# Kernel optimization log

Hardware: AMD Instinct MI355X
Metric: run time of the kernel (lower is better)

Reference implementation:

```python
import jax, jax.numpy as jnp
import numpy as np

D = 1024
H = 16
HS = 64

def setup_inputs() -> dict:
    key = jax.random.key(0)
    ks = jax.random.split(key, 9)
    s = 0.02
    x = jax.random.normal(ks[0], (2, 4096, D), dtype=jnp.float32)
    Wq = jax.random.normal(ks[1], (H, D, HS), dtype=jnp.float32) * s
    Wk = jax.random.normal(ks[2], (H, D, HS), dtype=jnp.float32) * s
    Wv = jax.random.normal(ks[3], (H, D, HS), dtype=jnp.float32) * s
    bq = jax.random.normal(ks[4], (H, HS), dtype=jnp.float32) * s
    bk = jax.random.normal(ks[5], (H, HS), dtype=jnp.float32) * s
    bv = jax.random.normal(ks[6], (H, HS), dtype=jnp.float32) * s
    Wp = jax.random.normal(ks[7], (D, D), dtype=jnp.float32) * s
    bp = jax.random.normal(ks[8], (D,), dtype=jnp.float32) * s
    return {"x": x, "Wq": Wq, "Wk": Wk, "Wv": Wv, "bq": bq, "bk": bk, "bv": bv, "Wp": Wp, "bp": bp}

def reference(x, Wq, Wk, Wv, bq, bk, bv, Wp, bp):
    B, T, _ = x.shape
    # per-head projections, stacked over heads: [B, H, T, HS]
    q = jnp.einsum('btd,hde->bhte', x, Wq) + bq[None, :, None, :]
    k = jnp.einsum('btd,hde->bhte', x, Wk) + bk[None, :, None, :]
    v = jnp.einsum('btd,hde->bhte', x, Wv) + bv[None, :, None, :]
    scale = 1.0 / jnp.sqrt(jnp.float32(HS))
    scores = jnp.einsum('bhte,bhse->bhts', q, k) * scale  # [B,H,T,T]
    causal = jnp.tril(jnp.ones((T, T), dtype=bool))
    scores = jnp.where(causal[None, None, :, :], scores, -jnp.inf)
    attn = jax.nn.softmax(scores, axis=-1)
    out = jnp.einsum('bhts,bhse->bhte', attn, v)  # [B,H,T,HS]
    # concat heads along last dim (head order preserved)
    out = out.transpose(0, 2, 1, 3).reshape(B, T, H * HS)
    return out @ Wp + bp
```

## Files before the change

kernel.cpp:

```cpp
#include <hip/hip_runtime.h>
#include <hip/hip_bf16.h>
#include <stdint.h>


typedef __bf16 bf16x8 __attribute__((ext_vector_type(8)));
typedef float f32x4 __attribute__((ext_vector_type(4)));
typedef float f32x16 __attribute__((ext_vector_type(16)));
typedef __attribute__((address_space(1))) void gvoid_t;
typedef __attribute__((address_space(3))) void lvoid_t;

using hbf = __hip_bfloat16;

#define QSCALE (0.125f * 1.44269504088896f)

static __device__ __forceinline__ void gload_lds16(const void* g, void* l) {
  __builtin_amdgcn_global_load_lds((gvoid_t*)g, (lvoid_t*)l, 16, 0, 0);
}

static __device__ __forceinline__ uint16_t b2u(float x) {
  hbf h = __float2bfloat16(x);
  return *reinterpret_cast<uint16_t*>(&h);
}

static __device__ __forceinline__ uint32_t cvtpk(float lo, float hi) {
  uint32_t r;
  asm("v_cvt_pk_bf16_f32 %0, %1, %2" : "=v"(r) : "v"(lo), "v"(hi));
  return r;
}

static __device__ __forceinline__ void pl32swap(uint32_t& x, uint32_t& y) {
  asm volatile("v_permlane32_swap_b32 %0, %1" : "+v"(x), "+v"(y));
}

static __device__ __forceinline__ float max3f(float a, float b, float c) {
  return fmaxf(fmaxf(a, b), c);
}


__global__ void k_cvt_all(const float* __restrict__ x,
                          const float* __restrict__ Wq, const float* __restrict__ Wk,
                          const float* __restrict__ Wv,
                          const float* __restrict__ bq, const float* __restrict__ bk,
                          const float* __restrict__ bv,
                          const float* __restrict__ Wp,
                          hbf* __restrict__ xb, hbf* __restrict__ Wt,
                          hbf* __restrict__ Wpt, float* __restrict__ biasc) {
  const int b = blockIdx.x, tid = threadIdx.x;
  if (b < 8192) {
    int i = (b * 256 + tid) * 4;
    float4 v = *reinterpret_cast<const float4*>(x + i);
    hbf h[4] = {__float2bfloat16(v.x), __float2bfloat16(v.y),
                __float2bfloat16(v.z), __float2bfloat16(v.w)};
    *reinterpret_cast<ushort4*>(xb + i) = *reinterpret_cast<ushort4*>(h);
  } else if (b < 20480) {
    int idx = (b - 8192) * 256 + tid;
    int d = idx & 1023, r = idx >> 10;
    int m = r >> 10, rem = r & 1023;
    int h = rem >> 6, e = rem & 63;
    const float* W = (m == 0) ? Wq : (m == 1) ? Wk : Wv;
    float v = W[(h << 10 | d) * 64 + e];
    if (m == 0) v *= QSCALE;
    Wt[idx] = __float2bfloat16(v);
  } else if (b < 24576) {
    int idx = (b - 20480) * 256 + tid;
    int o = idx >> 10, d = idx & 1023;
    Wpt[idx] = __float2bfloat16(Wp[(d << 10) + o]);
  } else {
    int r = (b - 24576) * 256 + tid;
    int m = r >> 10, rem = r & 1023;
    const float* bsrc = (m == 0) ? bq : (m == 1) ? bk : bv;
    float v = bsrc[rem];
    if (m == 0) v *= QSCALE;
    biasc[r] = v;
  }
}


__global__ __launch_bounds__(256) void k_gemm_qkv(
    const hbf* __restrict__ A, const hbf* __restrict__ Bw,
    const float* __restrict__ biasc, hbf* __restrict__ qkv) {
  __shared__ __align__(16) hbf sA[128 * 64];
  __shared__ __align__(16) hbf sB[128 * 64];
  const int tid = threadIdx.x;
  const int lane = tid & 63, wid = tid >> 6;
  int wg = blockIdx.y * 64 + blockIdx.x;
  wg = (wg & 7) * 192 + (wg >> 3);
  const int m0 = (wg & 63) * 128, n0 = (wg >> 6) * 128;
  const int g = lane >> 4, cl = lane & 15;

  const f32x4 fz = {0.f, 0.f, 0.f, 0.f};
  f32x4 acc[4][4];
#pragma unroll
  for (int a = 0; a < 4; ++a)
#pragma unroll
    for (int b = 0; b < 4; ++b) acc[a][b] = fz;

  const int srow = wid * 32 + (lane >> 3);
  const int scol = (lane & 7) * 8;

  for (int kt = 0; kt < 16; ++kt) {
    const int k0 = kt * 64;
#pragma unroll
    for (int t = 0; t < 4; ++t) {
      const int r = srow + t * 8;
      gload_lds16(A + (size_t)(m0 + r) * 1024 + k0 + scol, sA + (wid * 32 + t * 8) * 64);
      gload_lds16(Bw + (size_t)(n0 + r) * 1024 + k0 + scol, sB + (wid * 32 + t * 8) * 64);
    }
    __syncthreads();
#pragma unroll
    for (int ks = 0; ks < 2; ++ks) {
      const int ko = ks * 32 + g * 8;
      bf16x8 af[4], bfr[4];
#pragma unroll
      for (int rt = 0; rt < 4; ++rt)
        af[rt] = *reinterpret_cast<const bf16x8*>(sA + ((wid & 1) * 64 + rt * 16 + cl) * 64 + ko);
#pragma unroll
      for (int ct = 0; ct < 4; ++ct)
        bfr[ct] = *reinterpret_cast<const bf16x8*>(sB + ((wid >> 1) * 64 + ct * 16 + cl) * 64 + ko);
#pragma unroll
      for (int rt = 0; rt < 4; ++rt)
#pragma unroll
        for (int ct = 0; ct < 4; ++ct)
          acc[rt][ct] = __builtin_amdgcn_mfma_f32_16x16x32_bf16(af[rt], bfr[ct], acc[rt][ct], 0, 0, 0);
    }
    __syncthreads();
  }

#pragma unroll
  for (int rt = 0; rt < 4; ++rt)
#pragma unroll
    for (int ct = 0; ct < 4; ++ct) {
      const int colg = n0 + (wid >> 1) * 64 + ct * 16 + cl;
      const int mi = colg >> 10, rem = colg & 1023;
      const int h = rem >> 6, e = rem & 63;
      const float bi = biasc[colg];
      if (mi == 2) {
        const int t0 = m0 + (wid & 1) * 64 + rt * 16 + g * 4;
        const int b = t0 >> 12, t = t0 & 4095;
        ushort4 o;
        o.x = b2u(acc[rt][ct][0] + bi);
        o.y = b2u(acc[rt][ct][1] + bi);
        o.z = b2u(acc[rt][ct][2] + bi);
        o.w = b2u(acc[rt][ct][3] + bi);
        *reinterpret_cast<ushort4*>(
            qkv + (size_t)64 * 262144 + (size_t)(b * 16 + h) * 262144 + (size_t)e * 4096 + t) = o;
      } else {
#pragma unroll
        for (int i = 0; i < 4; ++i) {
          const int rowg = m0 + (wid & 1) * 64 + rt * 16 + g * 4 + i;
          const int b = rowg >> 12, t = rowg & 4095;
          qkv[(((size_t)mi * 32 + b * 16 + h) * 4096 + t) * 64 + e] =
              __float2bfloat16(acc[rt][ct][i] + bi);
        }
      }
    }
}


__global__ __launch_bounds__(256) void k_flash(
    const hbf* __restrict__ qkv, hbf* __restrict__ attn) {
  __shared__ __align__(16) __bf16 sK[2][64 * 64];
  __shared__ __align__(16) __bf16 sV[2][64 * 64];
  const int tid = threadIdx.x, lane = tid & 63, wq = tid >> 6;
  const int h = lane >> 5, r31 = lane & 31;
  const int bh = blockIdx.x;
  const int qtb = (int)gridDim.y - 1 - (int)blockIdx.y;
  const int q0 = qtb * 128;
  const int ntile = 2 * qtb + 2;
  const hbf* Q  = qkv + (size_t)bh * 262144;
  const hbf* Kp = qkv + (size_t)(32 + bh) * 262144;
  const hbf* Vp = qkv + (size_t)(64 + bh) * 262144;
  const float NEG_INF = -__builtin_inff();

  const int koff = (wq * 16 + (lane >> 3)) * 64 + (((lane & 7) ^ (lane >> 3)) * 8);
  const int voff = (wq * 16 + (lane >> 3)) * 4096 + (((lane & 7) ^ (lane >> 3)) * 8);

  const int qrow = q0 + wq * 32 + r31;
  bf16x8 aq[4];
#pragma unroll
  for (int ks = 0; ks < 4; ++ks)
    aq[ks] = *reinterpret_cast<const bf16x8*>(Q + (size_t)qrow * 64 + ks * 16 + h * 8);

  f32x16 accO[2];
#pragma unroll
  for (int et = 0; et < 2; ++et)
#pragma unroll
    for (int i = 0; i < 16; ++i) accO[et][i] = 0.f;
  float mrow = NEG_INF, lrow = 0.f;

  gload_lds16(Kp + koff,         &sK[0][wq * 1024]);
  gload_lds16(Kp + koff + 512,   &sK[0][wq * 1024 + 512]);
  gload_lds16(Vp + voff,         &sV[0][wq * 1024]);
  gload_lds16(Vp + voff + 32768, &sV[0][wq * 1024 + 512]);
  __syncthreads();

  const int qmaxw = q0 + wq * 32 + 31;
  int buf = 0;
  for (int jt = 0; jt < ntile; ++jt) {
    if (jt < ntile - 1) {
      const hbf* Kg = Kp + (size_t)(jt + 1) * 4096;
      gload_lds16(Kg + koff,       &sK[buf ^ 1][wq * 1024]);
      gload_lds16(Kg + koff + 512, &sK[buf ^ 1][wq * 1024 + 512]);
      const hbf* Vg = Vp + (jt + 1) * 64;
      gload_lds16(Vg + voff,         &sV[buf ^ 1][wq * 1024]);
      gload_lds16(Vg + voff + 32768, &sV[buf ^ 1][wq * 1024 + 512]);
    }

    if (64 * jt <= qmaxw) {
      const __bf16* sKb = sK[buf];
      const __bf16* sVb = sV[buf];

      f32x16 accS[2];
      __builtin_amdgcn_s_setprio(1);
#pragma unroll
      for (int t = 0; t < 2; ++t) {
        f32x16 s;
#pragma unroll
        for (int i = 0; i < 16; ++i) s[i] = 0.f;
#pragma unroll
        for (int ks = 0; ks < 4; ++ks) {
          bf16x8 ak = *reinterpret_cast<const bf16x8*>(
              sKb + (t * 32 + r31) * 64 + (((2 * ks + h) ^ (r31 & 7)) * 8));
          s = __builtin_amdgcn_mfma_f32_32x32x16_bf16(ak, aq[ks], s, 0, 0, 0);
        }
        accS[t] = s;
      }
      __builtin_amdgcn_s_setprio(0);

      if (64 * jt + 63 > q0 + wq * 32) {
#pragma unroll
        for (int t = 0; t < 2; ++t)
#pragma unroll
          for (int i = 0; i < 16; ++i) {
            const int kvg = 64 * jt + 32 * t + (i & 3) + 8 * (i >> 2) + 4 * h;
            if (kvg > qrow) accS[t][i] = NEG_INF;
          }
      }

      float g0 = max3f(accS[0][0], accS[0][1], accS[0][2]);
      float g1 = max3f(accS[0][3], accS[0][4], accS[0][5]);
      float g2 = max3f(accS[0][6], accS[0][7], accS[0][8]);
      float g3 = max3f(accS[0][9], accS[0][10], accS[0][11]);
      float g4 = max3f(accS[0][12], accS[0][13], accS[0][14]);
      float g5 = max3f(accS[0][15], accS[1][0], accS[1][1]);
      float g6 = max3f(accS[1][2], accS[1][3], accS[1][4]);
      float g7 = max3f(accS[1][5], accS[1][6], accS[1][7]);
      float g8 = max3f(accS[1][8], accS[1][9], accS[1][10]);
      float g9 = max3f(accS[1][11], accS[1][12], accS[1][13]);
      float gA = fmaxf(accS[1][14], accS[1][15]);
      float h0 = max3f(g0, g1, g2);
      float h1 = max3f(g3, g4, g5);
      float h2 = max3f(g6, g7, g8);
      float h3 = fmaxf(g9, gA);
      float pmax = fmaxf(max3f(h0, h1, h2), h3);
      pmax = fmaxf(pmax, __shfl_xor(pmax, 32));

      if (!__all(pmax - mrow <= 8.f)) {
        const float mn = fmaxf(mrow, pmax);
        const float corr = __builtin_amdgcn_exp2f(mrow - mn);
        mrow = mn;
        lrow *= corr;
#pragma unroll
        for (int et = 0; et < 2; ++et)
#pragma unroll
          for (int i = 0; i < 16; ++i) accO[et][i] *= corr;
      }

#pragma unroll
      for (int t = 0; t < 2; ++t)
#pragma unroll
        for (int i = 0; i < 16; ++i)
          accS[t][i] = __builtin_amdgcn_exp2f(accS[t][i] - mrow);
      float s0 = (accS[0][0] + accS[0][1]) + (accS[0][2] + accS[0][3]);
      float s1 = (accS[0][4] + accS[0][5]) + (accS[0][6] + accS[0][7]);
      float s2 = (accS[0][8] + accS[0][9]) + (accS[0][10] + accS[0][11]);
      float s3 = (accS[0][12] + accS[0][13]) + (accS[0][14] + accS[0][15]);
      float s4 = (accS[1][0] + accS[1][1]) + (accS[1][2] + accS[1][3]);
      float s5 = (accS[1][4] + accS[1][5]) + (accS[1][6] + accS[1][7]);
      float s6 = (accS[1][8] + accS[1][9]) + (accS[1][10] + accS[1][11]);
      float s7 = (accS[1][12] + accS[1][13]) + (accS[1][14] + accS[1][15]);
      float rs = ((s0 + s1) + (s2 + s3)) + ((s4 + s5) + (s6 + s7));
      rs += __shfl_xor(rs, 32);
      lrow += rs;

      uint32_t d0[2][4], d1[2][4];
#pragma unroll
      for (int t = 0; t < 2; ++t)
#pragma unroll
        for (int r4 = 0; r4 < 4; ++r4) {
          d0[t][r4] = cvtpk(accS[t][4 * r4 + 0], accS[t][4 * r4 + 1]);
          d1[t][r4] = cvtpk(accS[t][4 * r4 + 2], accS[t][4 * r4 + 3]);
        }

#pragma unroll
      for (int kb = 0; kb < 4; ++kb) {
        const int t = kb >> 1, ra = 2 * (kb & 1), rb = ra + 1;
        uint32_t x0 = d0[t][ra], y0 = d0[t][rb];
        uint32_t x1 = d1[t][ra], y1 = d1[t][rb];
        pl32swap(x0, y0);
        pl32swap(x1, y1);
        union { uint32_t u[4]; bf16x8 v; } bP;
        bP.u[0] = x0; bP.u[1] = x1; bP.u[2] = y0; bP.u[3] = y1;
        __builtin_amdgcn_s_setprio(1);
#pragma unroll
        for (int et = 0; et < 2; ++et) {
          bf16x8 av = *reinterpret_cast<const bf16x8*>(
              sVb + (et * 32 + r31) * 64 + (((2 * kb + h) ^ (r31 & 7)) * 8));
          accO[et] = __builtin_amdgcn_mfma_f32_32x32x16_bf16(av, bP.v, accO[et], 0, 0, 0);
        }
        __builtin_amdgcn_s_setprio(0);
      }
    }

    __syncthreads();
    buf ^= 1;
  }

  const float inv = 1.0f / lrow;
  hbf* arow = attn + ((size_t)(bh >> 4) * 4096 + qrow) * 1024 + (bh & 15) * 64;
#pragma unroll
  for (int et = 0; et < 2; ++et)
#pragma unroll
    for (int r4 = 0; r4 < 4; ++r4) {
      const int e0 = et * 32 + 8 * r4 + 4 * h;
      ushort4 o;
      o.x = b2u(accO[et][4 * r4 + 0] * inv);
      o.y = b2u(accO[et][4 * r4 + 1] * inv);
      o.z = b2u(accO[et][4 * r4 + 2] * inv);
      o.w = b2u(accO[et][4 * r4 + 3] * inv);
      *reinterpret_cast<ushort4*>(arow + e0) = o;
    }
}


__global__ __launch_bounds__(256) void k_gemm_out(
    const hbf* __restrict__ A, const hbf* __restrict__ Bw,
    const float* __restrict__ bp, float* __restrict__ out) {
  __shared__ __align__(16) hbf sA[128 * 64];
  __shared__ __align__(16) hbf sB[128 * 64];
  const int tid = threadIdx.x;
  const int lane = tid & 63, wid = tid >> 6;
  int wg = blockIdx.y * 64 + blockIdx.x;
  wg = (wg & 7) * 64 + (wg >> 3);
  const int m0 = (wg & 63) * 128, n0 = (wg >> 6) * 128;
  const int g = lane >> 4, cl = lane & 15;

  const f32x4 fz = {0.f, 0.f, 0.f, 0.f};
  f32x4 acc[4][4];
#pragma unroll
  for (int a = 0; a < 4; ++a)
#pragma unroll
    for (int b = 0; b < 4; ++b) acc[a][b] = fz;

  const int srow = wid * 32 + (lane >> 3);
  const int scol = (lane & 7) * 8;

  for (int kt = 0; kt < 16; ++kt) {
    const int k0 = kt * 64;
#pragma unroll
    for (int t = 0; t < 4; ++t) {
      const int r = srow + t * 8;
      gload_lds16(A + (size_t)(m0 + r) * 1024 + k0 + scol, sA + (wid * 32 + t * 8) * 64);
      gload_lds16(Bw + (size_t)(n0 + r) * 1024 + k0 + scol, sB + (wid * 32 + t * 8) * 64);
    }
    __syncthreads();
#pragma unroll
    for (int ks = 0; ks < 2; ++ks) {
      const int ko = ks * 32 + g * 8;
      bf16x8 af[4], bfr[4];
#pragma unroll
      for (int rt = 0; rt < 4; ++rt)
        af[rt] = *reinterpret_cast<const bf16x8*>(sA + ((wid & 1) * 64 + rt * 16 + cl) * 64 + ko);
#pragma unroll
      for (int ct = 0; ct < 4; ++ct)
        bfr[ct] = *reinterpret_cast<const bf16x8*>(sB + ((wid >> 1) * 64 + ct * 16 + cl) * 64 + ko);
#pragma unroll
      for (int rt = 0; rt < 4; ++rt)
#pragma unroll
        for (int ct = 0; ct < 4; ++ct)
          acc[rt][ct] = __builtin_amdgcn_mfma_f32_16x16x32_bf16(af[rt], bfr[ct], acc[rt][ct], 0, 0, 0);
    }
    __syncthreads();
  }

#pragma unroll
  for (int rt = 0; rt < 4; ++rt)
#pragma unroll
    for (int ct = 0; ct < 4; ++ct) {
      const int colg = n0 + (wid >> 1) * 64 + ct * 16 + cl;
      const float bi = bp[colg];
#pragma unroll
      for (int i = 0; i < 4; ++i) {
        const int rowg = m0 + (wid & 1) * 64 + rt * 16 + g * 4 + i;
        out[(size_t)rowg * 1024 + colg] = acc[rt][ct][i] + bi;
      }
    }
}


extern "C" void kernel_launch(void* const* d_in, const int* in_sizes, int n_in,
                              void* d_out, int out_size, void* d_ws, size_t ws_size,
                              hipStream_t stream) {
  const float* x  = (const float*)d_in[0];
  const float* Wq = (const float*)d_in[1];
  const float* Wk = (const float*)d_in[2];
  const float* Wv = (const float*)d_in[3];
  const float* bq = (const float*)d_in[4];
  const float* bk = (const float*)d_in[5];
  const float* bv = (const float*)d_in[6];
  const float* Wp = (const float*)d_in[7];
  const float* bp = (const float*)d_in[8];
  float* out = (float*)d_out;

  char* ws = (char*)d_ws;
  hbf*   xb    = (hbf*)ws;
  hbf*   Wt    = (hbf*)(ws + 16777216);
  hbf*   Wpt   = (hbf*)(ws + 16777216 + 6291456);
  float* biasc = (float*)(ws + 16777216 + 6291456 + 2097152);
  hbf*   qkv   = (hbf*)(ws + 16777216 + 6291456 + 2097152 + 16384);
  hbf*   attn  = xb;

  k_cvt_all<<<24588, 256, 0, stream>>>(x, Wq, Wk, Wv, bq, bk, bv, Wp,
                                       xb, Wt, Wpt, biasc);

  dim3 g1(64, 24); k_gemm_qkv<<<g1, 256, 0, stream>>>(xb, Wt, biasc, qkv);
  dim3 g2(32, 32); k_flash   <<<g2, 256, 0, stream>>>(qkv, attn);
  dim3 g3(64, 8);  k_gemm_out<<<g3, 256, 0, stream>>>(attn, Wpt, bp, out);
}
```

Before: 244.4 us.

## Double-buffer QKV GEMM with 128x256 tiles, swizzled LDS and interleaved prefetch

Rewrites the QKV projection GEMM to use 512-thread blocks computing 128x256 tiles, with double-buffered LDS fed by async global-to-LDS loads two k-steps ahead. LDS columns are XOR-swizzled to avoid bank conflicts. The prefetch of the next stage is spread across the MFMA groups, separated by barriers, and MFMA sections run at raised wave priority. It also drops the workgroup-index remapping in both GEMMs, which may reduce L2 locality, and the larger LDS footprint may lower occupancy.

```diff
diff --git a/kernel.cpp b/kernel.cpp
--- a/kernel.cpp
+++ b/kernel.cpp
@@ -76,17 +76,18 @@
 }
 
 
-__global__ __launch_bounds__(256) void k_gemm_qkv(
+__global__ __launch_bounds__(512) void k_gemm_qkv(
     const hbf* __restrict__ A, const hbf* __restrict__ Bw,
     const float* __restrict__ biasc, hbf* __restrict__ qkv) {
-  __shared__ __align__(16) hbf sA[128 * 64];
-  __shared__ __align__(16) hbf sB[128 * 64];
+  __shared__ __align__(16) hbf sA[2][128 * 64];
+  __shared__ __align__(16) hbf sB[2][256 * 64];
   const int tid = threadIdx.x;
-  const int lane = tid & 63, wid = tid >> 6;
-  int wg = blockIdx.y * 64 + blockIdx.x;
-  wg = (wg & 7) * 192 + (wg >> 3);
-  const int m0 = (wg & 63) * 128, n0 = (wg >> 6) * 128;
+  const int lane = tid & 63, w = tid >> 6;
+  const int wm = w >> 2, wn = w & 3;
   const int g = lane >> 4, cl = lane & 15;
+  const int m0 = blockIdx.x * 128, n0 = blockIdx.y * 256;
+
+  const int sr = tid >> 3, sc = tid & 7;
 
   const f32x4 fz = {0.f, 0.f, 0.f, 0.f};
   f32x4 acc[4][4];
@@ -95,62 +96,113 @@
 #pragma unroll
     for (int b = 0; b < 4; ++b) acc[a][b] = fz;
 
-  const int srow = wid * 32 + (lane >> 3);
-  const int scol = (lane & 7) * 8;
+#pragma unroll
+  for (int kt = 0; kt < 2; ++kt) {
+#pragma unroll
+    for (int s = 0; s < 2; ++s) {
+      const int row = s * 64 + sr;
+      gload_lds16(A + (size_t)(m0 + row) * 1024 + kt * 64 + ((sc ^ (row & 7)) * 8),
+                  &sA[kt][s * 4096 + tid * 8]);
+    }
+#pragma unroll
+    for (int s = 0; s < 4; ++s) {
+      const int row = s * 64 + sr;
+      gload_lds16(Bw + (size_t)(n0 + row) * 1024 + kt * 64 + ((sc ^ (row & 7)) * 8),
+                  &sB[kt][s * 4096 + tid * 8]);
+    }
+  }
+  asm volatile("s_waitcnt vmcnt(6)" ::: "memory");
+  __builtin_amdgcn_s_barrier();
 
   for (int kt = 0; kt < 16; ++kt) {
-    const int k0 = kt * 64;
-#pragma unroll
-    for (int t = 0; t < 4; ++t) {
-      const int r = srow + t * 8;
-      gload_lds16(A + (size_t)(m0 + r) * 1024 + k0 + scol, sA + (wid * 32 + t * 8) * 64);
-      gload_lds16(Bw + (size_t)(n0 + r) * 1024 + k0 + scol, sB + (wid * 32 + t * 8) * 64);
-    }
-    __syncthreads();
-#pragma unroll
-    for (int ks = 0; ks < 2; ++ks) {
-      const int ko = ks * 32 + g * 8;
-      bf16x8 af[4], bfr[4];
+    const int bi = kt & 1;
+    const bool st = (kt + 2) < 16;
+
+    bf16x8 af[4][2], bf[4][2];
+#pragma unroll
+    for (int rt = 0; rt < 4; ++rt)
+#pragma unroll
+      for (int ks = 0; ks < 2; ++ks)
+        af[rt][ks] = *reinterpret_cast<const bf16x8*>(
+            &sA[bi][(wm * 64 + rt * 16 + cl) * 64 + (((ks * 4 + g) ^ (cl & 7)) * 8)]);
+#pragma unroll
+    for (int ct = 0; ct < 4; ++ct)
+#pragma unroll
+      for (int ks = 0; ks < 2; ++ks)
+        bf[ct][ks] = *reinterpret_cast<const bf16x8*>(
+            &sB[bi][(wn * 64 + ct * 16 + cl) * 64 + (((ks * 4 + g) ^ (cl & 7)) * 8)]);
+    __builtin_amdgcn_s_barrier();
+    asm volatile("s_waitcnt lgkmcnt(0)" ::: "memory");
+    __builtin_amdgcn_sched_barrier(0);
+    __builtin_amdgcn_s_setprio(1);
+#pragma unroll
+    for (int rt = 0; rt < 4; ++rt)
+#pragma unroll
+      for (int ks = 0; ks < 2; ++ks)
+        acc[rt][0] = __builtin_amdgcn_mfma_f32_16x16x32_bf16(af[rt][ks], bf[0][ks], acc[rt][0], 0, 0, 0);
+    __builtin_amdgcn_s_setprio(0);
+    __builtin_amdgcn_s_barrier();
+
+#pragma unroll
+    for (int q = 1; q < 4; ++q) {
+      if (st) {
+        if (q == 1) {
+#pragma unroll
+          for (int s = 0; s < 2; ++s) {
+            const int row = s * 64 + sr;
+            gload_lds16(A + (size_t)(m0 + row) * 1024 + (kt + 2) * 64 + ((sc ^ (row & 7)) * 8),
+                        &sA[bi][s * 4096 + tid * 8]);
+          }
+        } else {
+#pragma unroll
+          for (int s2 = 0; s2 < 2; ++s2) {
+            const int s = (q - 2) * 2 + s2;
+            const int row = s * 64 + sr;
+            gload_lds16(Bw + (size_t)(n0 + row) * 1024 + (kt + 2) * 64 + ((sc ^ (row & 7)) * 8),
+                        &sB[bi][s * 4096 + tid * 8]);
+          }
+        }
+      }
+      __builtin_amdgcn_s_setprio(1);
 #pragma unroll
       for (int rt = 0; rt < 4; ++rt)
-        af[rt] = *reinterpret_cast<const bf16x8*>(sA + ((wid & 1) * 64 + rt * 16 + cl) * 64 + ko);
-#pragma unroll
-      for (int ct = 0; ct < 4; ++ct)
-        bfr[ct] = *reinterpret_cast<const bf16x8*>(sB + ((wid >> 1) * 64 + ct * 16 + cl) * 64 + ko);
-#pragma unroll
-      for (int rt = 0; rt < 4; ++rt)
-#pragma unroll
-        for (int ct = 0; ct < 4; ++ct)
-          acc[rt][ct] = __builtin_amdgcn_mfma_f32_16x16x32_bf16(af[rt], bfr[ct], acc[rt][ct], 0, 0, 0);
-    }
-    __syncthreads();
+#pragma unroll
+        for (int ks = 0; ks < 2; ++ks)
+          acc[rt][q] = __builtin_amdgcn_mfma_f32_16x16x32_bf16(af[rt][ks], bf[q][ks], acc[rt][q], 0, 0, 0);
+      __builtin_amdgcn_s_setprio(0);
+      if (q == 3) {
+        if (st) asm volatile("s_waitcnt vmcnt(6)" ::: "memory");
+        else    asm volatile("s_waitcnt vmcnt(0)" ::: "memory");
+      }
+      __builtin_amdgcn_s_barrier();
+    }
   }
 
 #pragma unroll
   for (int rt = 0; rt < 4; ++rt)
 #pragma unroll
     for (int ct = 0; ct < 4; ++ct) {
-      const int colg = n0 + (wid >> 1) * 64 + ct * 16 + cl;
+      const int colg = n0 + wn * 64 + ct * 16 + cl;
       const int mi = colg >> 10, rem = colg & 1023;
       const int h = rem >> 6, e = rem & 63;
-      const float bi = biasc[colg];
+      const float bi_ = biasc[colg];
       if (mi == 2) {
-        const int t0 = m0 + (wid & 1) * 64 + rt * 16 + g * 4;
+        const int t0 = m0 + wm * 64 + rt * 16 + g * 4;
         const int b = t0 >> 12, t = t0 & 4095;
         ushort4 o;
-        o.x = b2u(acc[rt][ct][0] + bi);
-        o.y = b2u(acc[rt][ct][1] + bi);
-        o.z = b2u(acc[rt][ct][2] + bi);
-        o.w = b2u(acc[rt][ct][3] + bi);
+        o.x = b2u(acc[rt][ct][0] + bi_);
+        o.y = b2u(acc[rt][ct][1] + bi_);
+        o.z = b2u(acc[rt][ct][2] + bi_);
+        o.w = b2u(acc[rt][ct][3] + bi_);
         *reinterpret_cast<ushort4*>(
             qkv + (size_t)64 * 262144 + (size_t)(b * 16 + h) * 262144 + (size_t)e * 4096 + t) = o;
       } else {
 #pragma unroll
         for (int i = 0; i < 4; ++i) {
-          const int rowg = m0 + (wid & 1) * 64 + rt * 16 + g * 4 + i;
+          const int rowg = m0 + wm * 64 + rt * 16 + g * 4 + i;
           const int b = rowg >> 12, t = rowg & 4095;
           qkv[(((size_t)mi * 32 + b * 16 + h) * 4096 + t) * 64 + e] =
-              __float2bfloat16(acc[rt][ct][i] + bi);
+              __float2bfloat16(acc[rt][ct][i] + bi_);
         }
       }
     }
@@ -340,9 +392,7 @@
   __shared__ __align__(16) hbf sB[128 * 64];
   const int tid = threadIdx.x;
   const int lane = tid & 63, wid = tid >> 6;
-  int wg = blockIdx.y * 64 + blockIdx.x;
-  wg = (wg & 7) * 64 + (wg >> 3);
-  const int m0 = (wg & 63) * 128, n0 = (wg >> 6) * 128;
+  const int m0 = blockIdx.x * 128, n0 = blockIdx.y * 128;
   const int g = lane >> 4, cl = lane & 15;
 
   const f32x4 fz = {0.f, 0.f, 0.f, 0.f};
@@ -423,7 +473,7 @@
   k_cvt_all<<<24588, 256, 0, stream>>>(x, Wq, Wk, Wv, bq, bk, bv, Wp,
                                        xb, Wt, Wpt, biasc);
 
-  dim3 g1(64, 24); k_gemm_qkv<<<g1, 256, 0, stream>>>(xb, Wt, biasc, qkv);
+  dim3 g1(64, 12); k_gemm_qkv<<<g1, 512, 0, stream>>>(xb, Wt, biasc, qkv);
   dim3 g2(32, 32); k_flash   <<<g2, 256, 0, stream>>>(qkv, attn);
   dim3 g3(64, 8);  k_gemm_out<<<g3, 256, 0, stream>>>(attn, Wpt, bp, out);
 }
```

After: 219.0 us. -10.4%, faster.
